# Optimization experiments

Hardware: AMD Instinct MI355X
Metric: run time of the kernel (lower is better)

The kernel has to match this reference:

```python
import jax, jax.numpy as jnp
import numpy as np

N = 50000   # nodes
E = 1600000 # edges
G = 512     # graphs in batch
IN_DIM, EMBED, H, D = 64, 128, 4, 32
D1, D2, D3 = 128, 64, 16
NEG_SLOPE = 0.2  # DGL GATConv default


def setup_inputs() -> dict:
    key = jax.random.key(0)
    ks = jax.random.split(key, 16)
    def glorot(k, shape):
        fan = shape[0] + shape[-1]
        return jax.random.normal(k, shape, jnp.float32) * jnp.sqrt(2.0 / fan)
    return {
        "feature": jax.random.normal(ks[0], (N, IN_DIM), jnp.float32),
        "src": jax.random.randint(ks[1], (E,), 0, N, jnp.int32),
        "dst": jax.random.randint(ks[2], (E,), 0, N, jnp.int32),
        "graph_ids": jnp.sort(jax.random.randint(ks[3], (N,), 0, G, jnp.int32)),
        "W0": glorot(ks[4], (IN_DIM, EMBED)), "b0": jnp.zeros((EMBED,), jnp.float32),
        "Wfc": glorot(ks[5], (EMBED, H * D)),
        "attn_l": glorot(ks[6], (H, D)), "attn_r": glorot(ks[7], (H, D)),
        "gat_bias": jnp.zeros((H * D,), jnp.float32),
        "W1": glorot(ks[8], (H * D, D1)), "b1": jnp.zeros((D1,), jnp.float32),
        "W2": glorot(ks[9], (D1, D2)), "b2": jnp.zeros((D2,), jnp.float32),
        "W3": glorot(ks[10], (D2, D3)), "b3": jnp.zeros((D3,), jnp.float32),
    }


def reference(feature, src, dst, graph_ids, W0, b0, Wfc, attn_l, attn_r,
              gat_bias, W1, b1, W2, b2, W3, b3):
    # initial dense embed
    h = feature @ W0 + b0                                   # [N, EMBED]
    # GATConv
    feat = (h @ Wfc).reshape(N, H, D)                       # [N,H,D]
    el = jnp.einsum('nhd,hd->nh', feat, attn_l)             # [N,H]
    er = jnp.einsum('nhd,hd->nh', feat, attn_r)
    e = jax.nn.leaky_relu(el[src] + er[dst], NEG_SLOPE)     # [E,H]
    # segment softmax over incoming edges of each dst node
    m = jax.ops.segment_max(e, dst, num_segments=N)         # [N,H]
    ex = jnp.exp(e - m[dst])                                # [E,H]
    denom = jax.ops.segment_sum(ex, dst, num_segments=N)    # [N,H]
    a = ex / denom[dst]                                     # [E,H]
    msg = a[:, :, None] * feat[src]                         # [E,H,D]
    rst = jax.ops.segment_sum(msg, dst, num_segments=N)     # [N,H,D]
    rst = rst + gat_bias.reshape(1, H, D)
    hn = rst.reshape(N, H * D)
    # AvgPooling per graph
    sums = jax.ops.segment_sum(hn, graph_ids, num_segments=G)           # [G,H*D]
    cnts = jax.ops.segment_sum(jnp.ones((N,), hn.dtype), graph_ids, num_segments=G)
    hg = sums / jnp.maximum(cnts, 1.0)[:, None]
    # dense head
    out = jax.nn.elu(hg)
    out = jax.nn.elu(out @ W1 + b1)
    out = jax.nn.elu(out @ W2 + b2)
    out = out @ W3 + b3                                     # [G, D3]
    atten = a[:, :, None]                                   # [E,H,1] like DGL
    return out, atten
```

## Files before the change

kernel.cpp:

```cpp
#include <hip/hip_runtime.h>
#include <hip/hip_fp16.h>
#include <math.h>

#define N_NODES 50000
#define E_EDGES 1600000
#define G_GRAPHS 512
#define IN_DIM 64
#define EMBED 128
#define HD 128
#define NHEAD 4
#define D1 128
#define D2 64
#define D3 16
#define NEG_SLOPE 0.2f
#define NB ((N_NODES + 127) >> 7)
#define PT_TILE 4096
#define PT_BLOCKS ((E_EDGES + PT_TILE - 1) / PT_TILE)
#define FB_CAP 8192

typedef float vfloat4 __attribute__((ext_vector_type(4)));
typedef float vfloat2 __attribute__((ext_vector_type(2)));
typedef unsigned short ushort_t;

static __device__ __forceinline__ float leaky(float x) { return x > 0.f ? x : NEG_SLOPE * x; }

__global__ void __launch_bounds__(256) k0hg(const int* __restrict__ dst, int* __restrict__ ghist,
                                            const float* __restrict__ W0, const float* __restrict__ b0,
                                            const float* __restrict__ Wfc, float* __restrict__ Wc,
                                            float* __restrict__ bc) {
    __shared__ int lh[NB];
    const int t = threadIdx.x;
    if (blockIdx.x < PT_BLOCKS) {
        for (int i = t; i < NB; i += 256) lh[i] = 0;
        __syncthreads();
        const long e0 = (long)blockIdx.x * PT_TILE;
#pragma unroll
        for (int k = 0; k < PT_TILE / 256; ++k) {
            long e = e0 + t + k * 256;
            if (e < E_EDGES) atomicAdd(&lh[dst[e] >> 7], 1);
        }
        __syncthreads();
        for (int i = t; i < NB; i += 256) {
            int v = lh[i];
            if (v) atomicAdd(&ghist[i], v);
        }
    } else {
        int tid = (int)(blockIdx.x - PT_BLOCKS) * 256 + t;
        if (tid < IN_DIM * HD) {
            int i = tid >> 7, j = tid & 127;
            float acc = 0.f;
            for (int k = 0; k < EMBED; ++k) acc += W0[i * EMBED + k] * Wfc[k * HD + j];
            Wc[tid] = acc;
        } else if (tid < IN_DIM * HD + HD) {
            int j = tid - IN_DIM * HD;
            float acc = 0.f;
            for (int k = 0; k < EMBED; ++k) acc += b0[k] * Wfc[k * HD + j];
            bc[j] = acc;
        }
    }
}

__global__ void __launch_bounds__(256) k1_gemm(const float* __restrict__ A,
                                               const float* __restrict__ W,
                                               const float* __restrict__ b,
                                               const float* __restrict__ attn_l,
                                               const float* __restrict__ attn_r,
                                               unsigned char* __restrict__ feat,
                                               float* __restrict__ el,
                                               float* __restrict__ er) {
    __shared__ __align__(16) float Ws[IN_DIM * HD];
    __shared__ __align__(16) float As[64][68];
    const int t = threadIdx.x;
    const int cc = t & 31;
    const int rt = t >> 5;
    const int c0 = cc * 4;
    const int r0 = rt * 8;
    const int row0 = blockIdx.x * 64;

    {
        const float4* Wg = (const float4*)W;
        float4* Wl = (float4*)Ws;
#pragma unroll
        for (int j = 0; j < (IN_DIM * HD / 4) / 256; ++j) Wl[t + j * 256] = Wg[t + j * 256];
    }
#pragma unroll
    for (int j = 0; j < 4; ++j) {
        int i2 = t + j * 256;
        int row = i2 >> 4, kq = i2 & 15;
        int gr = row0 + row;
        float4 v = (gr < N_NODES) ? *(const float4*)(A + (size_t)gr * IN_DIM + kq * 4)
                                  : make_float4(0.f, 0.f, 0.f, 0.f);
        *(float4*)&As[row][kq * 4] = v;
    }
    __syncthreads();

    float acc[8][4];
#pragma unroll
    for (int i = 0; i < 8; ++i)
#pragma unroll
        for (int j = 0; j < 4; ++j) acc[i][j] = 0.f;

    for (int k4 = 0; k4 < IN_DIM / 4; ++k4) {
        vfloat4 w0 = *(const vfloat4*)&Ws[(k4 * 4 + 0) * HD + c0];
        vfloat4 w1 = *(const vfloat4*)&Ws[(k4 * 4 + 1) * HD + c0];
        vfloat4 w2 = *(const vfloat4*)&Ws[(k4 * 4 + 2) * HD + c0];
        vfloat4 w3 = *(const vfloat4*)&Ws[(k4 * 4 + 3) * HD + c0];
#pragma unroll
        for (int i = 0; i < 8; ++i) {
            vfloat4 a = *(const vfloat4*)&As[r0 + i][k4 * 4];
#pragma unroll
            for (int j = 0; j < 4; ++j)
                acc[i][j] += a.x * w0[j] + a.y * w1[j] + a.z * w2[j] + a.w * w3[j];
        }
    }

    {
        vfloat4 bcv = *(const vfloat4*)(b + c0);
#pragma unroll
        for (int i = 0; i < 8; ++i)
#pragma unroll
            for (int j = 0; j < 4; ++j) acc[i][j] += bcv[j];
    }

#pragma unroll
    for (int i = 0; i < 8; ++i) {
        int gr = row0 + r0 + i;
        if (gr < N_NODES) {
            unsigned int ww = __builtin_amdgcn_cvt_pk_fp8_f32(acc[i][0], acc[i][1], 0, false);
            ww = __builtin_amdgcn_cvt_pk_fp8_f32(acc[i][2], acc[i][3], ww, true);
            *(unsigned int*)(feat + (size_t)gr * HD + c0) = ww;
        }
    }

    {
        vfloat4 al = *(const vfloat4*)(attn_l + c0);
        vfloat4 ar = *(const vfloat4*)(attn_r + c0);
        float pl[8], pr[8];
#pragma unroll
        for (int i = 0; i < 8; ++i) {
            pl[i] = acc[i][0] * al[0] + acc[i][1] * al[1] + acc[i][2] * al[2] + acc[i][3] * al[3];
            pr[i] = acc[i][0] * ar[0] + acc[i][1] * ar[1] + acc[i][2] * ar[2] + acc[i][3] * ar[3];
        }
#pragma unroll
        for (int off = 1; off <= 4; off <<= 1) {
#pragma unroll
            for (int i = 0; i < 8; ++i) {
                pl[i] += __shfl_xor(pl[i], off);
                pr[i] += __shfl_xor(pr[i], off);
            }
        }
        if ((cc & 7) == 0) {
            const int h = cc >> 3;
#pragma unroll
            for (int i = 0; i < 8; ++i) {
                int gr = row0 + r0 + i;
                if (gr < N_NODES) {
                    el[gr * 4 + h] = pl[i];
                    er[gr * 4 + h] = pr[i];
                }
            }
        }
    }
}

__global__ void __launch_bounds__(64) sc_scan(const int* __restrict__ ghist,
                                              int* __restrict__ coarse_start,
                                              int* __restrict__ cursorp) {
    const int lane = threadIdx.x;
    int run = 0;
    for (int c = 0; c < (NB + 63) / 64; ++c) {
        int i = c * 64 + lane;
        int v = (i < NB) ? ghist[i] : 0;
        int incl = v;
#pragma unroll
        for (int off = 1; off < 64; off <<= 1) {
            int o = __shfl_up(incl, off, 64);
            if (lane >= off) incl += o;
        }
        if (i < NB) {
            coarse_start[i] = run + incl - v;
            cursorp[i] = run + incl - v;
        }
        run += __shfl(incl, 63, 64);
    }
    if (lane == 0) coarse_start[NB] = E_EDGES;
}

__global__ void __launch_bounds__(256) pt_partition(const int* __restrict__ src,
                                                    const int* __restrict__ dst,
                                                    int* __restrict__ cursorp,
                                                    unsigned int* __restrict__ part) {
    __shared__ int hist[4][NB];
    __shared__ int tot[NB], offs[NB], base_s[NB];
    __shared__ int lcur[4][NB];
    __shared__ unsigned int stage[PT_TILE];
    const int t = threadIdx.x, lane = t & 63, wid = t >> 6;
    const long e0 = (long)blockIdx.x * PT_TILE;
    const int cnt = (int)min((long)PT_TILE, (long)E_EDGES - e0);
    for (int i = t; i < NB; i += 256) {
        hist[0][i] = 0; hist[1][i] = 0; hist[2][i] = 0; hist[3][i] = 0;
    }
    __syncthreads();
    unsigned int v[PT_TILE / 256];
#pragma unroll
    for (int k = 0; k < PT_TILE / 256; ++k) {
        int i = t + k * 256;
        if (i < cnt) {
            int d = dst[e0 + i];
            v[k] = ((unsigned int)d << 16) | (unsigned int)src[e0 + i];
            atomicAdd(&hist[wid][d >> 7], 1);
        } else v[k] = 0xFFFFFFFFu;
    }
    __syncthreads();
    for (int i = t; i < NB; i += 256) {
        int h0 = hist[0][i], h1 = hist[1][i], h2 = hist[2][i], h3 = hist[3][i];
        hist[0][i] = 0; hist[1][i] = h0; hist[2][i] = h0 + h1; hist[3][i] = h0 + h1 + h2;
        tot[i] = h0 + h1 + h2 + h3;
    }
    __syncthreads();
    if (wid == 0) {
        int run = 0;
        for (int c = 0; c < (NB + 63) / 64; ++c) {
            int i = c * 64 + lane;
            int vv = (i < NB) ? tot[i] : 0;
            int incl = vv;
#pragma unroll
            for (int off = 1; off < 64; off <<= 1) {
                int o = __shfl_up(incl, off, 64);
                if (lane >= off) incl += o;
            }
            if (i < NB) offs[i] = run + incl - vv;
            run += __shfl(incl, 63, 64);
        }
    }
    __syncthreads();
    for (int i = t; i < NB; i += 256) {
        int tt = tot[i];
        base_s[i] = tt ? atomicAdd(&cursorp[i], tt) : 0;
        int ob = offs[i];
        lcur[0][i] = ob + hist[0][i];
        lcur[1][i] = ob + hist[1][i];
        lcur[2][i] = ob + hist[2][i];
        lcur[3][i] = ob + hist[3][i];
    }
    __syncthreads();
#pragma unroll
    for (int k = 0; k < PT_TILE / 256; ++k) {
        if (v[k] != 0xFFFFFFFFu) {
            int b = v[k] >> 23;
            int pos = atomicAdd(&lcur[wid][b], 1);
            stage[pos] = v[k];
        }
    }
    __syncthreads();
    for (int i = t; i < cnt; i += 256) {
        unsigned int p = stage[i];
        int b = p >> 23;
        part[base_s[b] + (i - offs[b])] = p & 0x7FFFFFu;
    }
}

__global__ void __launch_bounds__(256) fb_fill(const unsigned int* __restrict__ part,
                                               const int* __restrict__ coarse_start,
                                               int* __restrict__ rowstart,
                                               ushort_t* __restrict__ csr_src) {
    const int b = blockIdx.x, t = threadIdx.x, lane = t & 63, wid = t >> 6;
    const int s0 = coarse_start[b], s1 = coarse_start[b + 1];
    const int cnt = s1 - s0;
    __shared__ int degl[4][128], totl[128], offl[128], curl[4][128];
    __shared__ ushort_t lsrc[FB_CAP];
    if (t < 128) { degl[0][t] = 0; degl[1][t] = 0; degl[2][t] = 0; degl[3][t] = 0; }
    __syncthreads();
    for (int i = t; i < cnt; i += 256) {
        unsigned int p = part[s0 + i];
        atomicAdd(&degl[wid][p >> 16], 1);
    }
    __syncthreads();
    if (t < 128) {
        int d0 = degl[0][t], d1 = degl[1][t], d2 = degl[2][t], d3 = degl[3][t];
        degl[0][t] = 0; degl[1][t] = d0; degl[2][t] = d0 + d1; degl[3][t] = d0 + d1 + d2;
        totl[t] = d0 + d1 + d2 + d3;
    }
    __syncthreads();
    if (wid == 0) {
        int run = 0;
        for (int c = 0; c < 2; ++c) {
            int i = c * 64 + lane;
            int vv = totl[i];
            int incl = vv;
#pragma unroll
            for (int off = 1; off < 64; off <<= 1) {
                int o = __shfl_up(incl, off, 64);
                if (lane >= off) incl += o;
            }
            offl[i] = run + incl - vv;
            run += __shfl(incl, 63, 64);
        }
    }
    __syncthreads();
    if (t < 128) {
        int ob = offl[t];
        curl[0][t] = ob + degl[0][t];
        curl[1][t] = ob + degl[1][t];
        curl[2][t] = ob + degl[2][t];
        curl[3][t] = ob + degl[3][t];
        int node = (b << 7) + t;
        if (node < N_NODES) rowstart[node] = s0 + ob;
    }
    if (b == 0 && t == 0) rowstart[N_NODES] = E_EDGES;
    __syncthreads();
    if (cnt <= FB_CAP) {
        for (int i = t; i < cnt; i += 256) {
            unsigned int p = part[s0 + i];
            int pos = atomicAdd(&curl[wid][p >> 16], 1);
            lsrc[pos] = (ushort_t)(p & 0xFFFFu);
        }
        __syncthreads();
        for (int i = t; i < cnt; i += 256) csr_src[s0 + i] = lsrc[i];
    } else {
        for (int i = t; i < cnt; i += 256) {
            unsigned int p = part[s0 + i];
            int pos = atomicAdd(&curl[wid][p >> 16], 1);
            csr_src[s0 + pos] = (ushort_t)(p & 0xFFFFu);
        }
    }
}

__global__ void __launch_bounds__(256) k6_aggregate(
    const ushort_t* __restrict__ csr_src, const int* __restrict__ rowstart,
    const float* __restrict__ el, const float* __restrict__ er,
    const unsigned char* __restrict__ feat, const float* __restrict__ gat_bias,
    float* __restrict__ er_rd, float* __restrict__ hn) {
    __shared__ uint2 s_pk[4][64][4];
    const int wid = threadIdx.x >> 6;
    const int lane = threadIdx.x & 63;
    const int n = blockIdx.x * 4 + wid;
    if (n >= N_NODES) return;
    const int start = rowstart[n];
    const int end = rowstart[n + 1];
    const int deg = end - start;

    const int e0 = lane >> 2;
    const int h = lane & 3;
    const float erh = er[n * 4 + h];
    float sm = 0.f;
    for (int base = 0; base < deg; base += 16) {
        const int e = base + e0;
        const bool v = e < deg;
        if (v) {
            const int s = csr_src[start + e];
            const float ex = __expf(leaky(el[s * 4 + h] + erh));
            sm += ex;
            if (e < 64)
                s_pk[wid][e][h] = make_uint2((unsigned int)s << 7, __float_as_uint(ex));
        }
    }
#pragma unroll
    for (int off = 4; off <= 32; off <<= 1) sm += __shfl_xor(sm, off);
    const float rd = sm > 0.f ? 1.f / sm : 0.f;
    if (lane < 4) {
        er_rd[(size_t)n * 8 + lane] = erh;
        er_rd[(size_t)n * 8 + 4 + lane] = rd;
    }

    const int g4 = lane >> 4, gl = lane & 15;
    const int h2 = gl >> 2;
    const float rdh = __shfl(rd, h2);
    vfloat2 acc0 = {0.f, 0.f}, acc1 = {0.f, 0.f}, acc2 = {0.f, 0.f}, acc3 = {0.f, 0.f};

    if (deg <= 64) {
        const uint2* pk = &s_pk[wid][0][h2];
        const unsigned char* fg = feat + (gl << 3);
        int idx = g4;
        for (; idx + 4 < deg; idx += 8) {
            const uint2 pA = pk[idx * 4];
            const uint2 pB = pk[(idx + 4) * 4];
            const uint2 wA = *(const uint2*)(fg + pA.x);
            const uint2 wB = *(const uint2*)(fg + pB.x);
            const float exA = __uint_as_float(pA.y);
            const float exB = __uint_as_float(pB.y);
            const vfloat2 eA = {exA, exA}, eB = {exB, exB};
            acc0 += eA * __builtin_amdgcn_cvt_pk_f32_fp8(wA.x, false);
            acc1 += eA * __builtin_amdgcn_cvt_pk_f32_fp8(wA.x, true);
            acc2 += eA * __builtin_amdgcn_cvt_pk_f32_fp8(wA.y, false);
            acc3 += eA * __builtin_amdgcn_cvt_pk_f32_fp8(wA.y, true);
            acc0 += eB * __builtin_amdgcn_cvt_pk_f32_fp8(wB.x, false);
            acc1 += eB * __builtin_amdgcn_cvt_pk_f32_fp8(wB.x, true);
            acc2 += eB * __builtin_amdgcn_cvt_pk_f32_fp8(wB.y, false);
            acc3 += eB * __builtin_amdgcn_cvt_pk_f32_fp8(wB.y, true);
        }
        if (idx < deg) {
            const uint2 p = pk[idx * 4];
            const uint2 w = *(const uint2*)(fg + p.x);
            const float ex = __uint_as_float(p.y);
            const vfloat2 ev = {ex, ex};
            acc0 += ev * __builtin_amdgcn_cvt_pk_f32_fp8(w.x, false);
            acc1 += ev * __builtin_amdgcn_cvt_pk_f32_fp8(w.x, true);
            acc2 += ev * __builtin_amdgcn_cvt_pk_f32_fp8(w.y, false);
            acc3 += ev * __builtin_amdgcn_cvt_pk_f32_fp8(w.y, true);
        }
    } else {
        const float erh2 = __shfl(erh, h2);
        const unsigned char* fg = feat + (gl << 3);
        for (int e = start + g4; e < end; e += 4) {
            const unsigned int s = csr_src[e];
            const float ex = __expf(leaky(el[s * 4 + h2] + erh2));
            const vfloat2 ev = {ex, ex};
            const uint2 w = *(const uint2*)(fg + ((size_t)s << 7));
            acc0 += ev * __builtin_amdgcn_cvt_pk_f32_fp8(w.x, false);
            acc1 += ev * __builtin_amdgcn_cvt_pk_f32_fp8(w.x, true);
            acc2 += ev * __builtin_amdgcn_cvt_pk_f32_fp8(w.y, false);
            acc3 += ev * __builtin_amdgcn_cvt_pk_f32_fp8(w.y, true);
        }
    }
    {
        const vfloat2 rv = {rdh, rdh};
        acc0 *= rv; acc1 *= rv; acc2 *= rv; acc3 *= rv;
    }
#pragma unroll
    for (int off = 16; off <= 32; off <<= 1) {
        acc0.x += __shfl_xor(acc0.x, off);
        acc0.y += __shfl_xor(acc0.y, off);
        acc1.x += __shfl_xor(acc1.x, off);
        acc1.y += __shfl_xor(acc1.y, off);
        acc2.x += __shfl_xor(acc2.x, off);
        acc2.y += __shfl_xor(acc2.y, off);
        acc3.x += __shfl_xor(acc3.x, off);
        acc3.y += __shfl_xor(acc3.y, off);
    }
    if (lane < 16) {
        const float4 b0 = ((const float4*)gat_bias)[gl * 2];
        const float4 b1 = ((const float4*)gat_bias)[gl * 2 + 1];
        float4* hp = (float4*)(hn + (size_t)n * HD + gl * 8);
        hp[0] = make_float4(acc0.x + b0.x, acc0.y + b0.y, acc1.x + b0.z, acc1.y + b0.w);
        hp[1] = make_float4(acc2.x + b1.x, acc2.y + b1.y, acc3.x + b1.z, acc3.y + b1.w);
    }
}

__global__ void __launch_bounds__(256) k6b_attn(
    const int* __restrict__ src, const int* __restrict__ dst,
    const float* __restrict__ el, const float* __restrict__ er_rd,
    float* __restrict__ a_out) {
    int e = blockIdx.x * 256 + threadIdx.x;
    if (e >= E_EDGES) return;
    const int s = src[e], d = dst[e];
    const float4 el4 = *(const float4*)(el + s * 4);
    const float4 er4 = *(const float4*)(er_rd + (size_t)d * 8);
    const float4 r4 = *(const float4*)(er_rd + (size_t)d * 8 + 4);
    vfloat4 a;
    a.x = __expf(leaky(el4.x + er4.x)) * r4.x;
    a.y = __expf(leaky(el4.y + er4.y)) * r4.y;
    a.z = __expf(leaky(el4.z + er4.z)) * r4.z;
    a.w = __expf(leaky(el4.w + er4.w)) * r4.w;
    __builtin_nontemporal_store(a, (vfloat4*)a_out + e);
}

__global__ void __launch_bounds__(512) k7_pool_mlp(
    const float* __restrict__ hn, const int* __restrict__ graph_ids,
    const float* __restrict__ W1, const float* __restrict__ b1,
    const float* __restrict__ W2, const float* __restrict__ b2,
    const float* __restrict__ W3, const float* __restrict__ b3,
    float* __restrict__ out) {
    const int g = blockIdx.x, t = threadIdx.x;
    const int tt = t & 127, part = t >> 7;
    __shared__ int bounds[2];
    __shared__ double pool[4][128];
    __shared__ double x[128], y[128];
    if (t < 2) {
        const int target = g + t;
        int lo = 0, hi = N_NODES;
        while (lo < hi) {
            int mid = (lo + hi) >> 1;
            if (graph_ids[mid] < target) lo = mid + 1; else hi = mid;
        }
        bounds[t] = lo;
    }
    __syncthreads();
    const int lo = bounds[0], hi = bounds[1];
    double s = 0.0;
    for (int n = lo + part; n < hi; n += 4) s += (double)hn[(size_t)n * HD + tt];
    pool[part][tt] = s;
    __syncthreads();
    if (t < 128) {
        const double cnt = (double)(hi - lo);
        const double sum = pool[0][t] + pool[1][t] + pool[2][t] + pool[3][t];
        const double v = sum / fmax(cnt, 1.0);
        x[t] = v > 0.0 ? v : expm1(v);
    }
    __syncthreads();
    if (t < 128) {
        double acc = (double)b1[t];
        for (int k = 0; k < HD; ++k) acc += x[k] * (double)W1[k * D1 + t];
        y[t] = acc > 0.0 ? acc : expm1(acc);
    }
    __syncthreads();
    if (t < D2) {
        double a2 = (double)b2[t];
        for (int k = 0; k < D1; ++k) a2 += y[k] * (double)W2[k * D2 + t];
        x[t] = a2 > 0.0 ? a2 : expm1(a2);
    }
    __syncthreads();
    if (t < D3) {
        double a3 = (double)b3[t];
        for (int k = 0; k < D2; ++k) a3 += x[k] * (double)W3[k * D3 + t];
        out[g * D3 + t] = (float)a3;
    }
}

extern "C" void kernel_launch(void* const* d_in, const int* in_sizes, int n_in,
                              void* d_out, int out_size, void* d_ws, size_t ws_size,
                              hipStream_t stream) {
    const float* feature = (const float*)d_in[0];
    const int* src = (const int*)d_in[1];
    const int* dst = (const int*)d_in[2];
    const int* graph_ids = (const int*)d_in[3];
    const float* W0 = (const float*)d_in[4];
    const float* b0 = (const float*)d_in[5];
    const float* Wfc = (const float*)d_in[6];
    const float* attn_l = (const float*)d_in[7];
    const float* attn_r = (const float*)d_in[8];
    const float* gat_bias = (const float*)d_in[9];
    const float* W1 = (const float*)d_in[10];
    const float* b1 = (const float*)d_in[11];
    const float* W2 = (const float*)d_in[12];
    const float* b2 = (const float*)d_in[13];
    const float* W3 = (const float*)d_in[14];
    const float* b3 = (const float*)d_in[15];

    char* ws = (char*)d_ws;
    size_t off = 0;
    auto carve = [&](size_t bytes) -> void* {
        void* p = ws + off;
        off += (bytes + 255) & ~(size_t)255;
        return p;
    };
    int* ghist = (int*)carve((size_t)NB * 4);
    const size_t zero_span = off;
    int* coarse_start = (int*)carve((size_t)(NB + 1) * 4);
    int* cursorp = (int*)carve((size_t)NB * 4);
    float* Wc = (float*)carve((size_t)IN_DIM * HD * 4);
    float* bc = (float*)carve((size_t)HD * 4);
    unsigned char* feat = (unsigned char*)carve((size_t)N_NODES * HD);
    float* el = (float*)carve((size_t)N_NODES * 4 * 4);
    float* er = (float*)carve((size_t)N_NODES * 4 * 4);
    float* er_rd = (float*)carve((size_t)N_NODES * 8 * 4);
    int* rowstart = (int*)carve((size_t)(N_NODES + 1) * 4);
    unsigned int* part = (unsigned int*)carve((size_t)E_EDGES * 4);
    ushort_t* csr_src = (ushort_t*)carve((size_t)E_EDGES * 2);

    float* out = (float*)d_out;
    float* hn = out + G_GRAPHS * D3;
    float* a_out = hn;

    (void)hipMemsetAsync(d_ws, 0, zero_span, stream);
    k0hg<<<PT_BLOCKS + 33, 256, 0, stream>>>(dst, ghist, W0, b0, Wfc, Wc, bc);
    k1_gemm<<<(N_NODES + 63) / 64, 256, 0, stream>>>(feature, Wc, bc, attn_l, attn_r,
                                                     feat, el, er);
    sc_scan<<<1, 64, 0, stream>>>(ghist, coarse_start, cursorp);
    pt_partition<<<PT_BLOCKS, 256, 0, stream>>>(src, dst, cursorp, part);
    fb_fill<<<NB, 256, 0, stream>>>(part, coarse_start, rowstart, csr_src);
    k6_aggregate<<<(N_NODES + 3) / 4, 256, 0, stream>>>(csr_src, rowstart, el, er, feat,
                                                        gat_bias, er_rd, hn);
    k7_pool_mlp<<<G_GRAPHS, 512, 0, stream>>>(hn, graph_ids, W1, b1, W2, b2, W3, b3, out);
    k6b_attn<<<(E_EDGES + 255) / 256, 256, 0, stream>>>(src, dst, el, er_rd, a_out);
}
```

Measured before the change: 250.4 us.

## Replace global atomic histogram and scan kernel with per-block histogram matrix

The edge-bucket histogram now writes per-block counts to a matrix instead of atomically adding into a global histogram. Each partition block recomputes the column sums, exclusive scan and its own prefix offset, which removes the memset, the single-block scan launch and the atomic cursor reservation. The attention-output kernel and the pool+MLP kernel are merged into one launch, with two graphs per block. This cuts launches and makes the partition deterministic, but every partition block now redundantly reads the whole histogram matrix (about 391x391 ints), and each graph's pooling loop is serial per thread.

```diff
diff --git a/kernel.cpp b/kernel.cpp
--- a/kernel.cpp
+++ b/kernel.cpp
@@ -17,6 +17,7 @@
 #define PT_TILE 4096
 #define PT_BLOCKS ((E_EDGES + PT_TILE - 1) / PT_TILE)
 #define FB_CAP 8192
+#define K6B_NBLK ((E_EDGES + 255) / 256)
 
 typedef float vfloat4 __attribute__((ext_vector_type(4)));
 typedef float vfloat2 __attribute__((ext_vector_type(2)));
@@ -24,10 +25,13 @@
 
 static __device__ __forceinline__ float leaky(float x) { return x > 0.f ? x : NEG_SLOPE * x; }
 
-__global__ void __launch_bounds__(256) k0hg(const int* __restrict__ dst, int* __restrict__ ghist,
-                                            const float* __restrict__ W0, const float* __restrict__ b0,
-                                            const float* __restrict__ Wfc, float* __restrict__ Wc,
-                                            float* __restrict__ bc) {
+__global__ void __launch_bounds__(256) m1_hist_wc(const int* __restrict__ dst,
+                                                  const float* __restrict__ W0,
+                                                  const float* __restrict__ b0,
+                                                  const float* __restrict__ Wfc,
+                                                  int* __restrict__ histM,
+                                                  float* __restrict__ Wc,
+                                                  float* __restrict__ bc) {
     __shared__ int lh[NB];
     const int t = threadIdx.x;
     if (blockIdx.x < PT_BLOCKS) {
@@ -40,10 +44,7 @@
             if (e < E_EDGES) atomicAdd(&lh[dst[e] >> 7], 1);
         }
         __syncthreads();
-        for (int i = t; i < NB; i += 256) {
-            int v = lh[i];
-            if (v) atomicAdd(&ghist[i], v);
-        }
+        for (int i = t; i < NB; i += 256) histM[(size_t)blockIdx.x * NB + i] = lh[i];
     } else {
         int tid = (int)(blockIdx.x - PT_BLOCKS) * 256 + t;
         if (tid < IN_DIM * HD) {
@@ -71,10 +72,8 @@
     __shared__ __align__(16) float Ws[IN_DIM * HD];
     __shared__ __align__(16) float As[64][68];
     const int t = threadIdx.x;
-    const int cc = t & 31;
-    const int rt = t >> 5;
-    const int c0 = cc * 4;
-    const int r0 = rt * 8;
+    const int cc = t & 31, rt = t >> 5;
+    const int c0 = cc * 4, r0 = rt * 8;
     const int row0 = blockIdx.x * 64;
 
     {
@@ -113,7 +112,6 @@
                 acc[i][j] += a.x * w0[j] + a.y * w1[j] + a.z * w2[j] + a.w * w3[j];
         }
     }
-
     {
         vfloat4 bcv = *(const vfloat4*)(b + c0);
 #pragma unroll
@@ -121,7 +119,6 @@
 #pragma unroll
             for (int j = 0; j < 4; ++j) acc[i][j] += bcv[j];
     }
-
 #pragma unroll
     for (int i = 0; i < 8; ++i) {
         int gr = row0 + r0 + i;
@@ -131,7 +128,6 @@
             *(unsigned int*)(feat + (size_t)gr * HD + c0) = ww;
         }
     }
-
     {
         vfloat4 al = *(const vfloat4*)(attn_l + c0);
         vfloat4 ar = *(const vfloat4*)(attn_r + c0);
@@ -163,44 +159,50 @@
     }
 }
 
-__global__ void __launch_bounds__(64) sc_scan(const int* __restrict__ ghist,
-                                              int* __restrict__ coarse_start,
-                                              int* __restrict__ cursorp) {
-    const int lane = threadIdx.x;
-    int run = 0;
-    for (int c = 0; c < (NB + 63) / 64; ++c) {
-        int i = c * 64 + lane;
-        int v = (i < NB) ? ghist[i] : 0;
-        int incl = v;
-#pragma unroll
-        for (int off = 1; off < 64; off <<= 1) {
-            int o = __shfl_up(incl, off, 64);
-            if (lane >= off) incl += o;
-        }
-        if (i < NB) {
-            coarse_start[i] = run + incl - v;
-            cursorp[i] = run + incl - v;
-        }
-        run += __shfl(incl, 63, 64);
-    }
-    if (lane == 0) coarse_start[NB] = E_EDGES;
-}
-
 __global__ void __launch_bounds__(256) pt_partition(const int* __restrict__ src,
                                                     const int* __restrict__ dst,
-                                                    int* __restrict__ cursorp,
-                                                    unsigned int* __restrict__ part) {
+                                                    const int* __restrict__ histM,
+                                                    unsigned int* __restrict__ part,
+                                                    int* __restrict__ coarse_start) {
     __shared__ int hist[4][NB];
     __shared__ int tot[NB], offs[NB], base_s[NB];
     __shared__ int lcur[4][NB];
+    __shared__ int gtot[NB], gpf[NB], offsG[NB];
     __shared__ unsigned int stage[PT_TILE];
     const int t = threadIdx.x, lane = t & 63, wid = t >> 6;
-    const long e0 = (long)blockIdx.x * PT_TILE;
+    const int blk = (int)blockIdx.x;
+    const long e0 = (long)blk * PT_TILE;
     const int cnt = (int)min((long)PT_TILE, (long)E_EDGES - e0);
+
+    for (int i = t; i < NB; i += 256) {
+        int cs = 0, pf = 0;
+        for (int bp = 0; bp < PT_BLOCKS; ++bp) {
+            int v = histM[(size_t)bp * NB + i];
+            cs += v;
+            if (bp < blk) pf += v;
+        }
+        gtot[i] = cs;
+        gpf[i] = pf;
+    }
     for (int i = t; i < NB; i += 256) {
         hist[0][i] = 0; hist[1][i] = 0; hist[2][i] = 0; hist[3][i] = 0;
     }
     __syncthreads();
+    if (wid == 0) {
+        int run = 0;
+        for (int c = 0; c < (NB + 63) / 64; ++c) {
+            int i = c * 64 + lane;
+            int v = (i < NB) ? gtot[i] : 0;
+            int incl = v;
+#pragma unroll
+            for (int off = 1; off < 64; off <<= 1) {
+                int o = __shfl_up(incl, off, 64);
+                if (lane >= off) incl += o;
+            }
+            if (i < NB) offsG[i] = run + incl - v;
+            run += __shfl(incl, 63, 64);
+        }
+    }
     unsigned int v[PT_TILE / 256];
 #pragma unroll
     for (int k = 0; k < PT_TILE / 256; ++k) {
@@ -212,6 +214,10 @@
         } else v[k] = 0xFFFFFFFFu;
     }
     __syncthreads();
+    if (t == 0) {
+        coarse_start[blk] = offsG[blk];
+        if (blk == 0) coarse_start[NB] = E_EDGES;
+    }
     for (int i = t; i < NB; i += 256) {
         int h0 = hist[0][i], h1 = hist[1][i], h2 = hist[2][i], h3 = hist[3][i];
         hist[0][i] = 0; hist[1][i] = h0; hist[2][i] = h0 + h1; hist[3][i] = h0 + h1 + h2;
@@ -235,8 +241,7 @@
     }
     __syncthreads();
     for (int i = t; i < NB; i += 256) {
-        int tt = tot[i];
-        base_s[i] = tt ? atomicAdd(&cursorp[i], tt) : 0;
+        base_s[i] = offsG[i] + gpf[i];
         int ob = offs[i];
         lcur[0][i] = ob + hist[0][i];
         lcur[1][i] = ob + hist[1][i];
@@ -346,8 +351,7 @@
     float sm = 0.f;
     for (int base = 0; base < deg; base += 16) {
         const int e = base + e0;
-        const bool v = e < deg;
-        if (v) {
+        if (e < deg) {
             const int s = csr_src[start + e];
             const float ex = __expf(leaky(el[s * 4 + h] + erh));
             sm += ex;
@@ -437,73 +441,68 @@
     }
 }
 
-__global__ void __launch_bounds__(256) k6b_attn(
+__global__ void __launch_bounds__(256) m2_attn_mlp(
     const int* __restrict__ src, const int* __restrict__ dst,
     const float* __restrict__ el, const float* __restrict__ er_rd,
-    float* __restrict__ a_out) {
-    int e = blockIdx.x * 256 + threadIdx.x;
-    if (e >= E_EDGES) return;
-    const int s = src[e], d = dst[e];
-    const float4 el4 = *(const float4*)(el + s * 4);
-    const float4 er4 = *(const float4*)(er_rd + (size_t)d * 8);
-    const float4 r4 = *(const float4*)(er_rd + (size_t)d * 8 + 4);
-    vfloat4 a;
-    a.x = __expf(leaky(el4.x + er4.x)) * r4.x;
-    a.y = __expf(leaky(el4.y + er4.y)) * r4.y;
-    a.z = __expf(leaky(el4.z + er4.z)) * r4.z;
-    a.w = __expf(leaky(el4.w + er4.w)) * r4.w;
-    __builtin_nontemporal_store(a, (vfloat4*)a_out + e);
-}
-
-__global__ void __launch_bounds__(512) k7_pool_mlp(
     const float* __restrict__ hn, const int* __restrict__ graph_ids,
     const float* __restrict__ W1, const float* __restrict__ b1,
     const float* __restrict__ W2, const float* __restrict__ b2,
     const float* __restrict__ W3, const float* __restrict__ b3,
-    float* __restrict__ out) {
-    const int g = blockIdx.x, t = threadIdx.x;
-    const int tt = t & 127, part = t >> 7;
-    __shared__ int bounds[2];
-    __shared__ double pool[4][128];
-    __shared__ double x[128], y[128];
-    if (t < 2) {
-        const int target = g + t;
-        int lo = 0, hi = N_NODES;
-        while (lo < hi) {
-            int mid = (lo + hi) >> 1;
-            if (graph_ids[mid] < target) lo = mid + 1; else hi = mid;
-        }
-        bounds[t] = lo;
-    }
-    __syncthreads();
-    const int lo = bounds[0], hi = bounds[1];
-    double s = 0.0;
-    for (int n = lo + part; n < hi; n += 4) s += (double)hn[(size_t)n * HD + tt];
-    pool[part][tt] = s;
-    __syncthreads();
-    if (t < 128) {
-        const double cnt = (double)(hi - lo);
-        const double sum = pool[0][t] + pool[1][t] + pool[2][t] + pool[3][t];
-        const double v = sum / fmax(cnt, 1.0);
-        x[t] = v > 0.0 ? v : expm1(v);
-    }
-    __syncthreads();
-    if (t < 128) {
-        double acc = (double)b1[t];
-        for (int k = 0; k < HD; ++k) acc += x[k] * (double)W1[k * D1 + t];
-        y[t] = acc > 0.0 ? acc : expm1(acc);
-    }
-    __syncthreads();
-    if (t < D2) {
-        double a2 = (double)b2[t];
-        for (int k = 0; k < D1; ++k) a2 += y[k] * (double)W2[k * D2 + t];
-        x[t] = a2 > 0.0 ? a2 : expm1(a2);
-    }
-    __syncthreads();
-    if (t < D3) {
-        double a3 = (double)b3[t];
-        for (int k = 0; k < D2; ++k) a3 += x[k] * (double)W3[k * D3 + t];
-        out[g * D3 + t] = (float)a3;
+    float* __restrict__ a_out, float* __restrict__ out) {
+    const int t = threadIdx.x;
+    if (blockIdx.x < K6B_NBLK) {
+        const long e = (long)blockIdx.x * 256 + t;
+        if (e >= E_EDGES) return;
+        const int s = src[e], d = dst[e];
+        const float4 el4 = *(const float4*)(el + s * 4);
+        const float4 er4 = *(const float4*)(er_rd + (size_t)d * 8);
+        const float4 r4 = *(const float4*)(er_rd + (size_t)d * 8 + 4);
+        vfloat4 a;
+        a.x = __expf(leaky(el4.x + er4.x)) * r4.x;
+        a.y = __expf(leaky(el4.y + er4.y)) * r4.y;
+        a.z = __expf(leaky(el4.z + er4.z)) * r4.z;
+        a.w = __expf(leaky(el4.w + er4.w)) * r4.w;
+        __builtin_nontemporal_store(a, (vfloat4*)a_out + e);
+    } else {
+        const int pair = (int)blockIdx.x - K6B_NBLK;
+        const int sub = t >> 7, tt = t & 127;
+        __shared__ int boundsg[3];
+        __shared__ double xg[2][128], yg[2][128];
+        if (t < 3) {
+            const int target = pair * 2 + t;
+            int lo = 0, hi = N_NODES;
+            while (lo < hi) {
+                int mid = (lo + hi) >> 1;
+                if (graph_ids[mid] < target) lo = mid + 1; else hi = mid;
+            }
+            boundsg[t] = lo;
+        }
+        __syncthreads();
+        const int lo = boundsg[sub], hi = boundsg[sub + 1];
+        double s = 0.0;
+        for (int n = lo; n < hi; ++n) s += (double)hn[(size_t)n * HD + tt];
+        {
+            const double v = s / fmax((double)(hi - lo), 1.0);
+            xg[sub][tt] = v > 0.0 ? v : expm1(v);
+        }
+        __syncthreads();
+        {
+            double acc = (double)b1[tt];
+            for (int k = 0; k < HD; ++k) acc += xg[sub][k] * (double)W1[k * D1 + tt];
+            yg[sub][tt] = acc > 0.0 ? acc : expm1(acc);
+        }
+        __syncthreads();
+        if (tt < D2) {
+            double a2 = (double)b2[tt];
+            for (int k = 0; k < D1; ++k) a2 += yg[sub][k] * (double)W2[k * D2 + tt];
+            xg[sub][tt] = a2 > 0.0 ? a2 : expm1(a2);
+        }
+        __syncthreads();
+        if (tt < D3) {
+            double a3 = (double)b3[tt];
+            for (int k = 0; k < D2; ++k) a3 += xg[sub][k] * (double)W3[k * D3 + tt];
+            out[(pair * 2 + sub) * D3 + tt] = (float)a3;
+        }
     }
 }
 
@@ -534,10 +533,8 @@
         off += (bytes + 255) & ~(size_t)255;
         return p;
     };
-    int* ghist = (int*)carve((size_t)NB * 4);
-    const size_t zero_span = off;
+    int* histM = (int*)carve((size_t)PT_BLOCKS * NB * 4);
     int* coarse_start = (int*)carve((size_t)(NB + 1) * 4);
-    int* cursorp = (int*)carve((size_t)NB * 4);
     float* Wc = (float*)carve((size_t)IN_DIM * HD * 4);
     float* bc = (float*)carve((size_t)HD * 4);
     unsigned char* feat = (unsigned char*)carve((size_t)N_NODES * HD);
@@ -547,20 +544,19 @@
     int* rowstart = (int*)carve((size_t)(N_NODES + 1) * 4);
     unsigned int* part = (unsigned int*)carve((size_t)E_EDGES * 4);
     ushort_t* csr_src = (ushort_t*)carve((size_t)E_EDGES * 2);
+    float* hn = (float*)carve((size_t)N_NODES * HD * 4);
 
     float* out = (float*)d_out;
-    float* hn = out + G_GRAPHS * D3;
-    float* a_out = hn;
-
-    (void)hipMemsetAsync(d_ws, 0, zero_span, stream);
-    k0hg<<<PT_BLOCKS + 33, 256, 0, stream>>>(dst, ghist, W0, b0, Wfc, Wc, bc);
+    float* a_out = out + G_GRAPHS * D3;
+
+    m1_hist_wc<<<PT_BLOCKS + 33, 256, 0, stream>>>(dst, W0, b0, Wfc, histM, Wc, bc);
     k1_gemm<<<(N_NODES + 63) / 64, 256, 0, stream>>>(feature, Wc, bc, attn_l, attn_r,
                                                      feat, el, er);
-    sc_scan<<<1, 64, 0, stream>>>(ghist, coarse_start, cursorp);
-    pt_partition<<<PT_BLOCKS, 256, 0, stream>>>(src, dst, cursorp, part);
+    pt_partition<<<PT_BLOCKS, 256, 0, stream>>>(src, dst, histM, part, coarse_start);
     fb_fill<<<NB, 256, 0, stream>>>(part, coarse_start, rowstart, csr_src);
     k6_aggregate<<<(N_NODES + 3) / 4, 256, 0, stream>>>(csr_src, rowstart, el, er, feat,
                                                         gat_bias, er_rd, hn);
-    k7_pool_mlp<<<G_GRAPHS, 512, 0, stream>>>(hn, graph_ids, W1, b1, W2, b2, W3, b3, out);
-    k6b_attn<<<(E_EDGES + 255) / 256, 256, 0, stream>>>(src, dst, el, er_rd, a_out);
-}
+    m2_attn_mlp<<<K6B_NBLK + G_GRAPHS / 2, 256, 0, stream>>>(src, dst, el, er_rd, hn,
+                                                             graph_ids, W1, b1, W2, b2,
+                                                             W3, b3, a_out, out);
+}
```

Result: slower. 287.3 us (+14.7%).

## Drop scan kernel and merge pool-MLP with attention output into one launch

Applied to the files above, without the earlier changes.

Removes the single-block sc_scan kernel. pt_partition now computes the global bucket offsets redundantly in each block from ghist, and fb_fill derives its range by summing ghist prefixes. The pooling/MLP kernel and the per-edge attention kernel are fused into one launch, with graph blocks first and edge blocks after. hn moves from the output buffer into the workspace so both halves can run at the same time. This cuts two launches and their serialization gaps, at the cost of redundant prefix-sum work in every partition and fill block.

```diff
diff --git a/kernel.cpp b/kernel.cpp
--- a/kernel.cpp
+++ b/kernel.cpp
@@ -17,6 +17,7 @@
 #define PT_TILE 4096
 #define PT_BLOCKS ((E_EDGES + PT_TILE - 1) / PT_TILE)
 #define FB_CAP 8192
+#define M2_EDGE_BLK ((E_EDGES + 511) / 512)
 
 typedef float vfloat4 __attribute__((ext_vector_type(4)));
 typedef float vfloat2 __attribute__((ext_vector_type(2)));
@@ -71,10 +72,8 @@
     __shared__ __align__(16) float Ws[IN_DIM * HD];
     __shared__ __align__(16) float As[64][68];
     const int t = threadIdx.x;
-    const int cc = t & 31;
-    const int rt = t >> 5;
-    const int c0 = cc * 4;
-    const int r0 = rt * 8;
+    const int cc = t & 31, rt = t >> 5;
+    const int c0 = cc * 4, r0 = rt * 8;
     const int row0 = blockIdx.x * 64;
 
     {
@@ -113,7 +112,6 @@
                 acc[i][j] += a.x * w0[j] + a.y * w1[j] + a.z * w2[j] + a.w * w3[j];
         }
     }
-
     {
         vfloat4 bcv = *(const vfloat4*)(b + c0);
 #pragma unroll
@@ -121,7 +119,6 @@
 #pragma unroll
             for (int j = 0; j < 4; ++j) acc[i][j] += bcv[j];
     }
-
 #pragma unroll
     for (int i = 0; i < 8; ++i) {
         int gr = row0 + r0 + i;
@@ -131,7 +128,6 @@
             *(unsigned int*)(feat + (size_t)gr * HD + c0) = ww;
         }
     }
-
     {
         vfloat4 al = *(const vfloat4*)(attn_l + c0);
         vfloat4 ar = *(const vfloat4*)(attn_r + c0);
@@ -163,42 +159,22 @@
     }
 }
 
-__global__ void __launch_bounds__(64) sc_scan(const int* __restrict__ ghist,
-                                              int* __restrict__ coarse_start,
-                                              int* __restrict__ cursorp) {
-    const int lane = threadIdx.x;
-    int run = 0;
-    for (int c = 0; c < (NB + 63) / 64; ++c) {
-        int i = c * 64 + lane;
-        int v = (i < NB) ? ghist[i] : 0;
-        int incl = v;
-#pragma unroll
-        for (int off = 1; off < 64; off <<= 1) {
-            int o = __shfl_up(incl, off, 64);
-            if (lane >= off) incl += o;
-        }
-        if (i < NB) {
-            coarse_start[i] = run + incl - v;
-            cursorp[i] = run + incl - v;
-        }
-        run += __shfl(incl, 63, 64);
-    }
-    if (lane == 0) coarse_start[NB] = E_EDGES;
-}
-
 __global__ void __launch_bounds__(256) pt_partition(const int* __restrict__ src,
                                                     const int* __restrict__ dst,
-                                                    int* __restrict__ cursorp,
+                                                    const int* __restrict__ ghist,
+                                                    int* __restrict__ cursor0,
                                                     unsigned int* __restrict__ part) {
     __shared__ int hist[4][NB];
     __shared__ int tot[NB], offs[NB], base_s[NB];
     __shared__ int lcur[4][NB];
+    __shared__ int gt[NB], offsG[NB];
     __shared__ unsigned int stage[PT_TILE];
     const int t = threadIdx.x, lane = t & 63, wid = t >> 6;
     const long e0 = (long)blockIdx.x * PT_TILE;
     const int cnt = (int)min((long)PT_TILE, (long)E_EDGES - e0);
     for (int i = t; i < NB; i += 256) {
         hist[0][i] = 0; hist[1][i] = 0; hist[2][i] = 0; hist[3][i] = 0;
+        gt[i] = ghist[i];
     }
     __syncthreads();
     unsigned int v[PT_TILE / 256];
@@ -232,11 +208,25 @@
             if (i < NB) offs[i] = run + incl - vv;
             run += __shfl(incl, 63, 64);
         }
+    } else if (wid == 1) {
+        int run = 0;
+        for (int c = 0; c < (NB + 63) / 64; ++c) {
+            int i = c * 64 + lane;
+            int vv = (i < NB) ? gt[i] : 0;
+            int incl = vv;
+#pragma unroll
+            for (int off = 1; off < 64; off <<= 1) {
+                int o = __shfl_up(incl, off, 64);
+                if (lane >= off) incl += o;
+            }
+            if (i < NB) offsG[i] = run + incl - vv;
+            run += __shfl(incl, 63, 64);
+        }
     }
     __syncthreads();
     for (int i = t; i < NB; i += 256) {
         int tt = tot[i];
-        base_s[i] = tt ? atomicAdd(&cursorp[i], tt) : 0;
+        base_s[i] = offsG[i] + (tt ? atomicAdd(&cursor0[i], tt) : 0);
         int ob = offs[i];
         lcur[0][i] = ob + hist[0][i];
         lcur[1][i] = ob + hist[1][i];
@@ -261,16 +251,30 @@
 }
 
 __global__ void __launch_bounds__(256) fb_fill(const unsigned int* __restrict__ part,
-                                               const int* __restrict__ coarse_start,
+                                               const int* __restrict__ ghist,
                                                int* __restrict__ rowstart,
                                                ushort_t* __restrict__ csr_src) {
     const int b = blockIdx.x, t = threadIdx.x, lane = t & 63, wid = t >> 6;
-    const int s0 = coarse_start[b], s1 = coarse_start[b + 1];
+    __shared__ int degl[4][128], totl[128], offl[128], curl[4][128];
+    __shared__ int red[4], s0s[2];
+    __shared__ ushort_t lsrc[FB_CAP];
+    {
+        int partial = 0;
+        for (int i = t; i < b; i += 256) partial += ghist[i];
+#pragma unroll
+        for (int off = 32; off; off >>= 1) partial += __shfl_xor(partial, off);
+        if (lane == 0) red[wid] = partial;
+        if (t < 128) { degl[0][t] = 0; degl[1][t] = 0; degl[2][t] = 0; degl[3][t] = 0; }
+        __syncthreads();
+        if (t == 0) {
+            int s0 = red[0] + red[1] + red[2] + red[3];
+            s0s[0] = s0;
+            s0s[1] = s0 + ghist[b];
+        }
+        __syncthreads();
+    }
+    const int s0 = s0s[0], s1 = s0s[1];
     const int cnt = s1 - s0;
-    __shared__ int degl[4][128], totl[128], offl[128], curl[4][128];
-    __shared__ ushort_t lsrc[FB_CAP];
-    if (t < 128) { degl[0][t] = 0; degl[1][t] = 0; degl[2][t] = 0; degl[3][t] = 0; }
-    __syncthreads();
     for (int i = t; i < cnt; i += 256) {
         unsigned int p = part[s0 + i];
         atomicAdd(&degl[wid][p >> 16], 1);
@@ -346,8 +350,7 @@
     float sm = 0.f;
     for (int base = 0; base < deg; base += 16) {
         const int e = base + e0;
-        const bool v = e < deg;
-        if (v) {
+        if (e < deg) {
             const int s = csr_src[start + e];
             const float ex = __expf(leaky(el[s * 4 + h] + erh));
             sm += ex;
@@ -437,73 +440,73 @@
     }
 }
 
-__global__ void __launch_bounds__(256) k6b_attn(
+__global__ void __launch_bounds__(512) m2b_mlp_attn(
     const int* __restrict__ src, const int* __restrict__ dst,
     const float* __restrict__ el, const float* __restrict__ er_rd,
-    float* __restrict__ a_out) {
-    int e = blockIdx.x * 256 + threadIdx.x;
-    if (e >= E_EDGES) return;
-    const int s = src[e], d = dst[e];
-    const float4 el4 = *(const float4*)(el + s * 4);
-    const float4 er4 = *(const float4*)(er_rd + (size_t)d * 8);
-    const float4 r4 = *(const float4*)(er_rd + (size_t)d * 8 + 4);
-    vfloat4 a;
-    a.x = __expf(leaky(el4.x + er4.x)) * r4.x;
-    a.y = __expf(leaky(el4.y + er4.y)) * r4.y;
-    a.z = __expf(leaky(el4.z + er4.z)) * r4.z;
-    a.w = __expf(leaky(el4.w + er4.w)) * r4.w;
-    __builtin_nontemporal_store(a, (vfloat4*)a_out + e);
-}
-
-__global__ void __launch_bounds__(512) k7_pool_mlp(
     const float* __restrict__ hn, const int* __restrict__ graph_ids,
     const float* __restrict__ W1, const float* __restrict__ b1,
     const float* __restrict__ W2, const float* __restrict__ b2,
     const float* __restrict__ W3, const float* __restrict__ b3,
-    float* __restrict__ out) {
-    const int g = blockIdx.x, t = threadIdx.x;
-    const int tt = t & 127, part = t >> 7;
-    __shared__ int bounds[2];
-    __shared__ double pool[4][128];
-    __shared__ double x[128], y[128];
-    if (t < 2) {
-        const int target = g + t;
-        int lo = 0, hi = N_NODES;
-        while (lo < hi) {
-            int mid = (lo + hi) >> 1;
-            if (graph_ids[mid] < target) lo = mid + 1; else hi = mid;
-        }
-        bounds[t] = lo;
-    }
-    __syncthreads();
-    const int lo = bounds[0], hi = bounds[1];
-    double s = 0.0;
-    for (int n = lo + part; n < hi; n += 4) s += (double)hn[(size_t)n * HD + tt];
-    pool[part][tt] = s;
-    __syncthreads();
-    if (t < 128) {
-        const double cnt = (double)(hi - lo);
-        const double sum = pool[0][t] + pool[1][t] + pool[2][t] + pool[3][t];
-        const double v = sum / fmax(cnt, 1.0);
-        x[t] = v > 0.0 ? v : expm1(v);
-    }
-    __syncthreads();
-    if (t < 128) {
-        double acc = (double)b1[t];
-        for (int k = 0; k < HD; ++k) acc += x[k] * (double)W1[k * D1 + t];
-        y[t] = acc > 0.0 ? acc : expm1(acc);
-    }
-    __syncthreads();
-    if (t < D2) {
-        double a2 = (double)b2[t];
-        for (int k = 0; k < D1; ++k) a2 += y[k] * (double)W2[k * D2 + t];
-        x[t] = a2 > 0.0 ? a2 : expm1(a2);
-    }
-    __syncthreads();
-    if (t < D3) {
-        double a3 = (double)b3[t];
-        for (int k = 0; k < D2; ++k) a3 += x[k] * (double)W3[k * D3 + t];
-        out[g * D3 + t] = (float)a3;
+    float* __restrict__ a_out, float* __restrict__ out) {
+    const int t = threadIdx.x;
+    if (blockIdx.x < G_GRAPHS) {
+        const int g = (int)blockIdx.x;
+        const int tt = t & 127, part = t >> 7;
+        __shared__ int bounds[2];
+        __shared__ double pool[4][128];
+        __shared__ double x[128], y[128];
+        if (t < 2) {
+            const int target = g + t;
+            int lo = 0, hi = N_NODES;
+            while (lo < hi) {
+                int mid = (lo + hi) >> 1;
+                if (graph_ids[mid] < target) lo = mid + 1; else hi = mid;
+            }
+            bounds[t] = lo;
+        }
+        __syncthreads();
+        const int lo = bounds[0], hi = bounds[1];
+        double s = 0.0;
+        for (int n = lo + part; n < hi; n += 4) s += (double)hn[(size_t)n * HD + tt];
+        pool[part][tt] = s;
+        __syncthreads();
+        if (t < 128) {
+            const double cnt = (double)(hi - lo);
+            const double sum = pool[0][t] + pool[1][t] + pool[2][t] + pool[3][t];
+            const double v = sum / fmax(cnt, 1.0);
+            x[t] = v > 0.0 ? v : expm1(v);
+        }
+        __syncthreads();
+        if (t < 128) {
+            double acc = (double)b1[t];
+            for (int k = 0; k < HD; ++k) acc += x[k] * (double)W1[k * D1 + t];
+            y[t] = acc > 0.0 ? acc : expm1(acc);
+        }
+        __syncthreads();
+        if (t < D2) {
+            double a2 = (double)b2[t];
+            for (int k = 0; k < D1; ++k) a2 += y[k] * (double)W2[k * D2 + t];
+            x[t] = a2 > 0.0 ? a2 : expm1(a2);
+        }
+        __syncthreads();
+        if (t < D3) {
+            double a3 = (double)b3[t];
+            for (int k = 0; k < D2; ++k) a3 += x[k] * (double)W3[k * D3 + t];
+            out[g * D3 + t] = (float)a3;
+        }
+    } else {
+        const long e = (long)(blockIdx.x - G_GRAPHS) * 512 + t;
+        if (e >= E_EDGES) return;
+        const int s = src[e], d = dst[e];
+        const float4 el4 = *(const float4*)(el + s * 4);
+        const float4 er4 = *(const float4*)(er_rd + (size_t)d * 8);
+        const float4 r4 = *(const float4*)(er_rd + (size_t)d * 8 + 4);
+        vfloat4 a;
+        a.x = __expf(leaky(el4.x + er4.x)) * r4.x;
+        a.y = __expf(leaky(el4.y + er4.y)) * r4.y;
+        a.z = __expf(leaky(el4.z + er4.z)) * r4.z;
+        a.w = __expf(leaky(el4.w + er4.w)) * r4.w;
+        __builtin_nontemporal_store(a, (vfloat4*)a_out + e);
     }
 }
 
@@ -535,9 +538,8 @@
         return p;
     };
     int* ghist = (int*)carve((size_t)NB * 4);
+    int* cursor0 = (int*)carve((size_t)NB * 4);
     const size_t zero_span = off;
-    int* coarse_start = (int*)carve((size_t)(NB + 1) * 4);
-    int* cursorp = (int*)carve((size_t)NB * 4);
     float* Wc = (float*)carve((size_t)IN_DIM * HD * 4);
     float* bc = (float*)carve((size_t)HD * 4);
     unsigned char* feat = (unsigned char*)carve((size_t)N_NODES * HD);
@@ -547,20 +549,20 @@
     int* rowstart = (int*)carve((size_t)(N_NODES + 1) * 4);
     unsigned int* part = (unsigned int*)carve((size_t)E_EDGES * 4);
     ushort_t* csr_src = (ushort_t*)carve((size_t)E_EDGES * 2);
+    float* hn = (float*)carve((size_t)N_NODES * HD * 4);
 
     float* out = (float*)d_out;
-    float* hn = out + G_GRAPHS * D3;
-    float* a_out = hn;
+    float* a_out = out + G_GRAPHS * D3;
 
     (void)hipMemsetAsync(d_ws, 0, zero_span, stream);
     k0hg<<<PT_BLOCKS + 33, 256, 0, stream>>>(dst, ghist, W0, b0, Wfc, Wc, bc);
     k1_gemm<<<(N_NODES + 63) / 64, 256, 0, stream>>>(feature, Wc, bc, attn_l, attn_r,
                                                      feat, el, er);
-    sc_scan<<<1, 64, 0, stream>>>(ghist, coarse_start, cursorp);
-    pt_partition<<<PT_BLOCKS, 256, 0, stream>>>(src, dst, cursorp, part);
-    fb_fill<<<NB, 256, 0, stream>>>(part, coarse_start, rowstart, csr_src);
+    pt_partition<<<PT_BLOCKS, 256, 0, stream>>>(src, dst, ghist, cursor0, part);
+    fb_fill<<<NB, 256, 0, stream>>>(part, ghist, rowstart, csr_src);
     k6_aggregate<<<(N_NODES + 3) / 4, 256, 0, stream>>>(csr_src, rowstart, el, er, feat,
                                                         gat_bias, er_rd, hn);
-    k7_pool_mlp<<<G_GRAPHS, 512, 0, stream>>>(hn, graph_ids, W1, b1, W2, b2, W3, b3, out);
-    k6b_attn<<<(E_EDGES + 255) / 256, 256, 0, stream>>>(src, dst, el, er_rd, a_out);
-}
+    m2b_mlp_attn<<<G_GRAPHS + M2_EDGE_BLK, 512, 0, stream>>>(src, dst, el, er_rd, hn,
+                                                             graph_ids, W1, b1, W2, b2,
+                                                             W3, b3, a_out, out);
+}
```

Result: faster. 234.3 us (-6.4%).
